# Kernel optimization log

Measured on AMD Instinct MI355X. Metric: run time of the kernel, lower is better.

Reference implementation:

```python
import jax, jax.numpy as jnp
import numpy as np

B, N, Q = 4, 4096, 4096
K = 32                    # max_neighbors (k = min(max_neighbors, N))
NUM_ATOM_TYPES = 100
EMBED_DIM = 32
RBF_DIM = 16
CUTOFF = 5.0
RBF_GAMMA = 1.0 / max(CUTOFF / max(RBF_DIM, 1), 1e-6) ** 2  # 10.24
EPS = 1e-12


def setup_inputs() -> dict:
    key = jax.random.key(0)
    k1, k2, k3, k4, k5 = jax.random.split(key, 5)
    coords = jax.random.normal(k1, (B, N, 3), dtype=jnp.float32) * 10.0
    atom_types = jax.random.randint(k2, (B, N), 0, NUM_ATOM_TYPES)
    radii = jax.random.uniform(k3, (B, N), dtype=jnp.float32) + 0.5
    query_points = jax.random.normal(k4, (B, Q, 3), dtype=jnp.float32) * 10.0
    atom_mask = jnp.ones((B, N), dtype=bool)
    query_mask = jnp.ones((B, Q), dtype=bool)
    embed_table = jax.random.normal(k5, (NUM_ATOM_TYPES, EMBED_DIM), dtype=jnp.float32)
    rbf_centers = jnp.linspace(0.0, CUTOFF, RBF_DIM, dtype=jnp.float32)
    return {"coords": coords, "atom_types": atom_types, "radii": radii,
            "query_points": query_points, "atom_mask": atom_mask,
            "query_mask": query_mask, "embed_table": embed_table,
            "rbf_centers": rbf_centers}


def reference(coords, atom_types, radii, query_points, atom_mask, query_mask,
              embed_table, rbf_centers):
    b = coords.shape[0]
    # stable pairwise distances [B, Q, N]
    diff = query_points[:, :, None, :] - coords[:, None, :, :]
    dists = jnp.sqrt(jnp.sum(diff * diff, axis=-1) + EPS)
    masked_dists = jnp.where(atom_mask[:, None, :], dists, jnp.inf)
    # smallest-k via top_k on negated distances -> [B, Q, K]
    neg_vals, sorted_indices = jax.lax.top_k(-masked_dists, K)
    sorted_dists = -neg_vals

    bidx = jnp.arange(b)[:, None, None]                       # [B,1,1]
    neighbor_atom_mask = atom_mask[bidx, sorted_indices]      # [B,Q,K]
    neighbor_mask = neighbor_atom_mask & (sorted_dists <= CUTOFF) & query_mask[:, :, None]

    neighbor_coords = coords[bidx, sorted_indices]            # [B,Q,K,3]
    neighbor_radii = radii[bidx, sorted_indices][..., None]   # [B,Q,K,1]
    neighbor_types = atom_types[bidx, sorted_indices]         # [B,Q,K]
    neighbor_emb = embed_table[neighbor_types]                # [B,Q,K,E]

    rel_pos = query_points[:, :, None, :] - neighbor_coords   # [B,Q,K,3]
    rel_dist = sorted_dists[..., None]                        # [B,Q,K,1]
    rbf = jnp.exp(-RBF_GAMMA * (rel_dist - rbf_centers[None, None, None, :]) ** 2)

    features = jnp.concatenate([rel_pos, neighbor_radii, neighbor_emb, rbf, rel_dist], axis=-1)
    features = jnp.where(neighbor_mask[..., None], features, 0.0)

    safe_indices = jnp.where(neighbor_atom_mask, sorted_indices, -1)
    safe_dists = jnp.where(neighbor_mask, sorted_dists, 0.0)
    return features, neighbor_mask, safe_indices, safe_dists
```

## Files before the change

### kernel.cpp

```cpp
#include <hip/hip_runtime.h>
#include <stdint.h>

#define B_ 4
#define N_ 4096
#define Q_ 4096
#define K_ 32
#define E_ 32
#define R_ 16
#define F_ 53

static constexpr int WAVES   = 16;
static constexpr int THREADS = WAVES * 64;
static constexpr int SUB     = 1024;
static constexpr int CAPL    = 352;
static constexpr int CAPT    = 64;
static constexpr int TILE    = K_ * F_;
static constexpr int NSLOT   = 4;
static constexpr int POOLB   = NSLOT * TILE * 4;

typedef float v2f __attribute__((ext_vector_type(2)));

__device__ __forceinline__ v2f pk_add(v2f a, v2f b) {
    v2f d; asm("v_pk_add_f32 %0, %1, %2" : "=v"(d) : "v"(a), "v"(b)); return d;
}
__device__ __forceinline__ v2f pk_mul(v2f a, v2f b) {
    v2f d; asm("v_pk_mul_f32 %0, %1, %2" : "=v"(d) : "v"(a), "v"(b)); return d;
}
__device__ __forceinline__ v2f pk_fma(v2f a, v2f b, v2f c) {
    v2f d; asm("v_pk_fma_f32 %0, %1, %2, %3" : "=v"(d) : "v"(a), "v"(b), "v"(c)); return d;
}
__device__ __forceinline__ v2f pk_s2(v2f qx, v2f qy, v2f qz,
                                     v2f nx, v2f ny, v2f nz) {
    const v2f dx = pk_add(qx, nx);
    const v2f dy = pk_add(qy, ny);
    const v2f dz = pk_add(qz, nz);
    return pk_fma(dz, dz, pk_fma(dy, dy, pk_mul(dx, dx)));
}
__device__ __forceinline__ float s2_fma(float qx, float qy, float qz,
                                        float nx, float ny, float nz) {
    const float dx = __fadd_rn(qx, nx);
    const float dy = __fadd_rn(qy, ny);
    const float dz = __fadd_rn(qz, nz);
    return __fmaf_rn(dz, dz, __fmaf_rn(dy, dy, __fmul_rn(dx, dx)));
}

__device__ __forceinline__ void bitonic_sort64_u32(unsigned int& v, int lane) {
    #pragma unroll
    for (int k = 2; k <= 64; k <<= 1) {
        #pragma unroll
        for (int j = k >> 1; j > 0; j >>= 1) {
            unsigned int o = __shfl_xor(v, j);
            const bool asc = ((lane & k) == 0);
            const bool lower = ((lane & j) == 0);
            unsigned int mn = v < o ? v : o;
            unsigned int mx = v < o ? o : v;
            v = (lower == asc) ? mn : mx;
        }
    }
}

__device__ __forceinline__ void bitonic_sort64_u64(unsigned long long& v, int lane) {
    #pragma unroll
    for (int k = 2; k <= 64; k <<= 1) {
        #pragma unroll
        for (int j = k >> 1; j > 0; j >>= 1) {
            unsigned long long o = __shfl_xor(v, j);
            const bool asc = ((lane & k) == 0);
            const bool lower = ((lane & j) == 0);
            unsigned long long mn = v < o ? v : o;
            unsigned long long mx = v < o ? o : v;
            v = (lower == asc) ? mn : mx;
        }
    }
}

__device__ __forceinline__ void merge64_u64(unsigned long long& best,
                                            unsigned long long c, int lane) {
    unsigned long long rev = __shfl(c, 63 - lane);
    unsigned long long v = best < rev ? best : rev;
    #pragma unroll
    for (int j = 32; j > 0; j >>= 1) {
        unsigned long long o = __shfl_xor(v, j);
        const bool lower = ((lane & j) == 0);
        unsigned long long mn = v < o ? v : o;
        unsigned long long mx = v < o ? o : v;
        v = lower ? mn : mx;
    }
    best = v;
}

__global__ __launch_bounds__(THREADS, 8)
void lfb_kernel(const float* __restrict__ coords,
                const int* __restrict__ atom_types,
                const float* __restrict__ radii,
                const float* __restrict__ qpts,
                const int* __restrict__ atom_mask,
                const int* __restrict__ query_mask,
                const float* __restrict__ embed,
                const float* __restrict__ centers,
                float* __restrict__ out)
{
    __shared__ __align__(16) float nsx[N_], nsy[N_], nsz[N_];
    __shared__ __align__(16) unsigned char pool[POOLB];

    const int tid  = threadIdx.x;
    const int lane = tid & 63;
    const int wv   = tid >> 6;
    const int bq0  = blockIdx.x * WAVES;
    const int b    = bq0 / Q_;

    for (int i = tid; i < N_; i += THREADS) {
        const float* c = coords + (size_t)(b * N_ + i) * 3;
        const bool mv = atom_mask[b * N_ + i] != 0;
        nsx[i] = mv ? -c[0] : -1e30f;
        nsy[i] = mv ? -c[1] : -1e30f;
        nsz[i] = mv ? -c[2] : -1e30f;
    }
    __syncthreads();

    const int bq = bq0 + wv;
    const float qx = qpts[(size_t)bq * 3 + 0];
    const float qy = qpts[(size_t)bq * 3 + 1];
    const float qz = qpts[(size_t)bq * 3 + 2];
    const v2f qx2 = {qx, qx}, qy2 = {qy, qy}, qz2 = {qz, qz};

    const float INFf = __uint_as_float(0x7F800000u);

    float l0 = INFf, l1 = INFf, l2 = INFf, l3 = INFf;
    for (int i = 0; i < SUB / 256; ++i) {
        const int a0 = i * 256 + lane * 4;
        const float4 X = *(const float4*)&nsx[a0];
        const float4 Y = *(const float4*)&nsy[a0];
        const float4 Z = *(const float4*)&nsz[a0];
        const v2f Xl = {X.x, X.y}, Xh = {X.z, X.w};
        const v2f Yl = {Y.x, Y.y}, Yh = {Y.z, Y.w};
        const v2f Zl = {Z.x, Z.y}, Zh = {Z.z, Z.w};
        const v2f sl = pk_s2(qx2, qy2, qz2, Xl, Yl, Zl);
        const v2f sh = pk_s2(qx2, qy2, qz2, Xh, Yh, Zh);
        l0 = fminf(l0, sl.x); l1 = fminf(l1, sl.y);
        l2 = fminf(l2, sh.x); l3 = fminf(l3, sh.y);
    }
    unsigned int tsl = __float_as_uint(fminf(fminf(l0, l1), fminf(l2, l3)));
    bitonic_sort64_u32(tsl, lane);
    const unsigned int STl = __shfl(tsl, 31) + 64u;

    unsigned int* loose = reinterpret_cast<unsigned int*>(pool) + wv * CAPL;
    unsigned int* tight = reinterpret_cast<unsigned int*>(pool)
                        + WAVES * CAPL + wv * CAPT;
    const unsigned long long lt = (1ull << lane) - 1ull;
    int cnt = 0;
    float m0 = INFf, m1 = INFf, m2 = INFf, m3 = INFf;
    auto collect = [&](float s, int idx) {
        const bool p = __float_as_uint(s) <= STl;
        const unsigned long long m = __ballot(p);
        if (p) {
            const int sl = cnt + __popcll(m & lt);
            if (sl < CAPL) loose[sl] = (unsigned int)idx;
        }
        cnt += __popcll(m);
    };
    for (int i = 0; i < N_ / 256; ++i) {
        const int a0 = i * 256 + lane * 4;
        const float4 X = *(const float4*)&nsx[a0];
        const float4 Y = *(const float4*)&nsy[a0];
        const float4 Z = *(const float4*)&nsz[a0];
        const v2f Xl = {X.x, X.y}, Xh = {X.z, X.w};
        const v2f Yl = {Y.x, Y.y}, Yh = {Y.z, Y.w};
        const v2f Zl = {Z.x, Z.y}, Zh = {Z.z, Z.w};
        const v2f sl = pk_s2(qx2, qy2, qz2, Xl, Yl, Zl);
        const v2f sh = pk_s2(qx2, qy2, qz2, Xh, Yh, Zh);
        m0 = fminf(m0, sl.x); m1 = fminf(m1, sl.y);
        m2 = fminf(m2, sh.x); m3 = fminf(m3, sh.y);
        collect(sl.x, a0 + 0);
        collect(sl.y, a0 + 1);
        collect(sh.x, a0 + 2);
        collect(sh.y, a0 + 3);
    }
    unsigned int tst = __float_as_uint(fminf(fminf(m0, m1), fminf(m2, m3)));
    bitonic_sort64_u32(tst, lane);
    const unsigned int STt = __shfl(tst, 31) + 64u;

    auto rekey = [&](int id) -> unsigned long long {
        const float dx = __fadd_rn(qx, nsx[id]);
        const float dy = __fadd_rn(qy, nsy[id]);
        const float dz = __fadd_rn(qz, nsz[id]);
        const float sv = __fadd_rn(
            __fadd_rn(__fmul_rn(dx, dx), __fmul_rn(dy, dy)),
            __fmul_rn(dz, dz));
        const float d = __fsqrt_rn(__fadd_rn(sv, 1e-12f));
        return ((unsigned long long)__float_as_uint(d) << 32) | (unsigned int)id;
    };

    unsigned long long key;
    if (cnt <= CAPL) {
        int tcnt = 0;
        const int nchL = (cnt + 63) >> 6;
        for (int c = 0; c < nchL; ++c) {
            const int slot = c * 64 + lane;
            const bool valid = slot < cnt;
            const int id = valid ? (int)loose[slot] : 0;
            const float s = s2_fma(qx, qy, qz, nsx[id], nsy[id], nsz[id]);
            const bool p = valid && (__float_as_uint(s) <= STt);
            const unsigned long long m = __ballot(p);
            if (p) {
                const int sl = tcnt + __popcll(m & lt);
                if (sl < CAPT) tight[sl] = (unsigned int)id;
            }
            tcnt += __popcll(m);
        }
        if (tcnt <= CAPT) {
            unsigned long long v = (lane < tcnt) ? rekey((int)tight[lane]) : ~0ull;
            bitonic_sort64_u64(v, lane);
            key = v;
        } else {
            unsigned long long best = ~0ull;
            for (int c = 0; c < nchL; ++c) {
                const int slot = c * 64 + lane;
                unsigned long long v =
                    (slot < cnt) ? rekey((int)loose[slot]) : ~0ull;
                bitonic_sort64_u64(v, lane);
                if (c == 0) best = v;
                else        merge64_u64(best, v, lane);
            }
            key = best;
        }
    } else {
        key = ~0ull;
        for (int base = 0; base < N_; base += 64) {
            const unsigned long long cand = rekey(base + lane);
            const unsigned long long T = __shfl(key, 31);
            unsigned long long m = __ballot(cand < T);
            while (m) {
                const int src = __ffsll(m) - 1;
                m &= m - 1;
                const unsigned long long nk = __shfl(cand, src);
                const unsigned long long up = __shfl_up(key, 1);
                if (lane < K_) {
                    const unsigned long long repl =
                        (lane == 0) ? nk : (up <= nk ? nk : up);
                    key = (key <= nk) ? key : repl;
                }
            }
        }
    }

    const size_t BQK = (size_t)B_ * Q_ * K_;
    float* out_feat = out;
    float* out_mask = out + BQK * (size_t)F_;
    float* out_idx  = out_mask + BQK;
    float* out_dist = out_idx + BQK;

    const bool qm = query_mask[bq] != 0;

    const float d_l  = __uint_as_float((unsigned int)(key >> 32));
    const int   id_l = (int)(key & 0xFFFFFFFFull) & (N_ - 1);
    const bool  am_l = ((unsigned int)(key >> 32)) < 0x7F800000u;
    const bool  nm_l = am_l && (d_l <= 5.0f) && qm;

    if (lane < K_) {
        const size_t o = (size_t)bq * K_ + lane;
        out_mask[o] = nm_l ? 1.0f : 0.0f;
        out_idx[o]  = am_l ? (float)id_l : -1.0f;
        out_dist[o] = nm_l ? d_l : 0.0f;
    }

    __syncthreads();

    float* stagef = reinterpret_cast<float*>(pool);
    for (int r = 0; r < WAVES / NSLOT; ++r) {
        if ((wv >> 2) == r) {
            float* f0 = stagef + (size_t)(wv & (NSLOT - 1)) * TILE;
            if (lane < K_) {
                float* f = f0 + lane * F_;
                f[0] = nm_l ? __fadd_rn(qx, nsx[id_l]) : 0.0f;
                f[1] = nm_l ? __fadd_rn(qy, nsy[id_l]) : 0.0f;
                f[2] = nm_l ? __fadd_rn(qz, nsz[id_l]) : 0.0f;
                f[3] = nm_l ? radii[b * N_ + id_l] : 0.0f;

                const int t = atom_types[b * N_ + id_l];
                const float4* er4 = (const float4*)(embed + t * E_);
                #pragma unroll
                for (int e = 0; e < E_ / 4; ++e) {
                    const float4 v = er4[e];
                    f[4 + e * 4 + 0] = nm_l ? v.x : 0.0f;
                    f[4 + e * 4 + 1] = nm_l ? v.y : 0.0f;
                    f[4 + e * 4 + 2] = nm_l ? v.z : 0.0f;
                    f[4 + e * 4 + 3] = nm_l ? v.w : 0.0f;
                }

                const float NG = -(float)(256.0 / 25.0);
                #pragma unroll
                for (int rr = 0; rr < R_; ++rr) {
                    const float dd = __fsub_rn(d_l, centers[rr]);
                    const float a2 = __fmul_rn(dd, dd);
                    f[36 + rr] = nm_l ? expf(__fmul_rn(NG, a2)) : 0.0f;
                }
                f[52] = nm_l ? d_l : 0.0f;
            }
            const float4* s4 = (const float4*)f0;
            float4* d4 = (float4*)(out_feat + (size_t)bq * (size_t)TILE);
            for (int t4 = lane; t4 < TILE / 4; t4 += 64) d4[t4] = s4[t4];
        }
        __syncthreads();
    }
}

extern "C" void kernel_launch(void* const* d_in, const int* in_sizes, int n_in,
                              void* d_out, int out_size, void* d_ws, size_t ws_size,
                              hipStream_t stream) {
    const float* coords     = (const float*)d_in[0];
    const int*   atom_types = (const int*)d_in[1];
    const float* radii      = (const float*)d_in[2];
    const float* qpts       = (const float*)d_in[3];
    const int*   atom_mask  = (const int*)d_in[4];
    const int*   query_mask = (const int*)d_in[5];
    const float* embed      = (const float*)d_in[6];
    const float* centers    = (const float*)d_in[7];

    dim3 grid((B_ * Q_) / WAVES);
    dim3 block(THREADS);
    lfb_kernel<<<grid, block, 0, stream>>>(coords, atom_types, radii, qpts,
                                           atom_mask, query_mask, embed, centers,
                                           (float*)d_out);
}
```

Before: 73.22 us.

## Replace two-stage ballot candidate filtering with exact full-scan threshold and per-lane buffers

```diff
diff --git a/kernel.cpp b/kernel.cpp
--- a/kernel.cpp
+++ b/kernel.cpp
@@ -11,12 +11,13 @@
 
 static constexpr int WAVES   = 16;
 static constexpr int THREADS = WAVES * 64;
-static constexpr int SUB     = 1024;
-static constexpr int CAPL    = 352;
-static constexpr int CAPT    = 64;
+static constexpr int CAP     = 6;
+static constexpr int CBUFW   = CAP * 64;
 static constexpr int TILE    = K_ * F_;
 static constexpr int NSLOT   = 4;
-static constexpr int POOLB   = NSLOT * TILE * 4;
+static constexpr int POOLU   = WAVES * CBUFW + WAVES * 64;
+static constexpr int POOLB   = (POOLU * 4 > NSLOT * TILE * 4)
+                             ? (POOLU * 4) : (NSLOT * TILE * 4);
 
 typedef float v2f __attribute__((ext_vector_type(2)));
 
@@ -35,13 +36,6 @@
     const v2f dy = pk_add(qy, ny);
     const v2f dz = pk_add(qz, nz);
     return pk_fma(dz, dz, pk_fma(dy, dy, pk_mul(dx, dx)));
-}
-__device__ __forceinline__ float s2_fma(float qx, float qy, float qz,
-                                        float nx, float ny, float nz) {
-    const float dx = __fadd_rn(qx, nx);
-    const float dy = __fadd_rn(qy, ny);
-    const float dz = __fadd_rn(qz, nz);
-    return __fmaf_rn(dz, dz, __fmaf_rn(dy, dy, __fmul_rn(dx, dx)));
 }
 
 __device__ __forceinline__ void bitonic_sort64_u32(unsigned int& v, int lane) {
@@ -72,21 +66,6 @@
             v = (lower == asc) ? mn : mx;
         }
     }
-}
-
-__device__ __forceinline__ void merge64_u64(unsigned long long& best,
-                                            unsigned long long c, int lane) {
-    unsigned long long rev = __shfl(c, 63 - lane);
-    unsigned long long v = best < rev ? best : rev;
-    #pragma unroll
-    for (int j = 32; j > 0; j >>= 1) {
-        unsigned long long o = __shfl_xor(v, j);
-        const bool lower = ((lane & j) == 0);
-        unsigned long long mn = v < o ? v : o;
-        unsigned long long mx = v < o ? o : v;
-        v = lower ? mn : mx;
-    }
-    best = v;
 }
 
 __global__ __launch_bounds__(THREADS, 8)
@@ -127,7 +106,7 @@
     const float INFf = __uint_as_float(0x7F800000u);
 
     float l0 = INFf, l1 = INFf, l2 = INFf, l3 = INFf;
-    for (int i = 0; i < SUB / 256; ++i) {
+    for (int i = 0; i < N_ / 256; ++i) {
         const int a0 = i * 256 + lane * 4;
         const float4 X = *(const float4*)&nsx[a0];
         const float4 Y = *(const float4*)&nsy[a0];
@@ -140,25 +119,16 @@
         l0 = fminf(l0, sl.x); l1 = fminf(l1, sl.y);
         l2 = fminf(l2, sh.x); l3 = fminf(l3, sh.y);
     }
-    unsigned int tsl = __float_as_uint(fminf(fminf(l0, l1), fminf(l2, l3)));
-    bitonic_sort64_u32(tsl, lane);
-    const unsigned int STl = __shfl(tsl, 31) + 64u;
-
-    unsigned int* loose = reinterpret_cast<unsigned int*>(pool) + wv * CAPL;
-    unsigned int* tight = reinterpret_cast<unsigned int*>(pool)
-                        + WAVES * CAPL + wv * CAPT;
-    const unsigned long long lt = (1ull << lane) - 1ull;
-    int cnt = 0;
-    float m0 = INFf, m1 = INFf, m2 = INFf, m3 = INFf;
-    auto collect = [&](float s, int idx) {
-        const bool p = __float_as_uint(s) <= STl;
-        const unsigned long long m = __ballot(p);
-        if (p) {
-            const int sl = cnt + __popcll(m & lt);
-            if (sl < CAPL) loose[sl] = (unsigned int)idx;
-        }
-        cnt += __popcll(m);
-    };
+    unsigned int mnb = __float_as_uint(fminf(fminf(l0, l1), fminf(l2, l3)));
+    bitonic_sort64_u32(mnb, lane);
+    const unsigned int Ts = __shfl(mnb, 31);
+    const bool degenerate = (Ts + 64u) >= 0x7F800000u;
+    const float STf = __uint_as_float(Ts + 64u);
+
+    unsigned int* poolu = reinterpret_cast<unsigned int*>(pool);
+    unsigned int* cbuf = poolu + wv * CBUFW;
+    unsigned int* comp = poolu + WAVES * CBUFW + wv * 64;
+    int cl = 0;
     for (int i = 0; i < N_ / 256; ++i) {
         const int a0 = i * 256 + lane * 4;
         const float4 X = *(const float4*)&nsx[a0];
@@ -169,16 +139,37 @@
         const v2f Zl = {Z.x, Z.y}, Zh = {Z.z, Z.w};
         const v2f sl = pk_s2(qx2, qy2, qz2, Xl, Yl, Zl);
         const v2f sh = pk_s2(qx2, qy2, qz2, Xh, Yh, Zh);
-        m0 = fminf(m0, sl.x); m1 = fminf(m1, sl.y);
-        m2 = fminf(m2, sh.x); m3 = fminf(m3, sh.y);
-        collect(sl.x, a0 + 0);
-        collect(sl.y, a0 + 1);
-        collect(sh.x, a0 + 2);
-        collect(sh.y, a0 + 3);
-    }
-    unsigned int tst = __float_as_uint(fminf(fminf(m0, m1), fminf(m2, m3)));
-    bitonic_sort64_u32(tst, lane);
-    const unsigned int STt = __shfl(tst, 31) + 64u;
+        {
+            const int s0 = cl < CAP ? cl : CAP - 1;
+            cbuf[s0 * 64 + lane] = (unsigned int)(a0 + 0);
+            cl += (sl.x <= STf) ? 1 : 0;
+        }
+        {
+            const int s1 = cl < CAP ? cl : CAP - 1;
+            cbuf[s1 * 64 + lane] = (unsigned int)(a0 + 1);
+            cl += (sl.y <= STf) ? 1 : 0;
+        }
+        {
+            const int s2 = cl < CAP ? cl : CAP - 1;
+            cbuf[s2 * 64 + lane] = (unsigned int)(a0 + 2);
+            cl += (sh.x <= STf) ? 1 : 0;
+        }
+        {
+            const int s3 = cl < CAP ? cl : CAP - 1;
+            cbuf[s3 * 64 + lane] = (unsigned int)(a0 + 3);
+            cl += (sh.y <= STf) ? 1 : 0;
+        }
+    }
+    const bool ovf = __ballot(cl >= CAP) != 0ull;
+
+    int x = cl;
+    #pragma unroll
+    for (int j = 1; j < 64; j <<= 1) {
+        const int t = __shfl_up(x, j);
+        if (lane >= j) x += t;
+    }
+    const int excl = x - cl;
+    const int tcnt = __shfl(x, 63);
 
     auto rekey = [&](int id) -> unsigned long long {
         const float dx = __fadd_rn(qx, nsx[id]);
@@ -192,38 +183,12 @@
     };
 
     unsigned long long key;
-    if (cnt <= CAPL) {
-        int tcnt = 0;
-        const int nchL = (cnt + 63) >> 6;
-        for (int c = 0; c < nchL; ++c) {
-            const int slot = c * 64 + lane;
-            const bool valid = slot < cnt;
-            const int id = valid ? (int)loose[slot] : 0;
-            const float s = s2_fma(qx, qy, qz, nsx[id], nsy[id], nsz[id]);
-            const bool p = valid && (__float_as_uint(s) <= STt);
-            const unsigned long long m = __ballot(p);
-            if (p) {
-                const int sl = tcnt + __popcll(m & lt);
-                if (sl < CAPT) tight[sl] = (unsigned int)id;
-            }
-            tcnt += __popcll(m);
-        }
-        if (tcnt <= CAPT) {
-            unsigned long long v = (lane < tcnt) ? rekey((int)tight[lane]) : ~0ull;
-            bitonic_sort64_u64(v, lane);
-            key = v;
-        } else {
-            unsigned long long best = ~0ull;
-            for (int c = 0; c < nchL; ++c) {
-                const int slot = c * 64 + lane;
-                unsigned long long v =
-                    (slot < cnt) ? rekey((int)loose[slot]) : ~0ull;
-                bitonic_sort64_u64(v, lane);
-                if (c == 0) best = v;
-                else        merge64_u64(best, v, lane);
-            }
-            key = best;
-        }
+    if (!degenerate && !ovf && tcnt <= 64) {
+        for (int j = 0; j < cl; ++j) comp[excl + j] = cbuf[j * 64 + lane];
+        unsigned long long v = ~0ull;
+        if (lane < tcnt) v = rekey((int)comp[lane]);
+        bitonic_sort64_u64(v, lane);
+        key = v;
     } else {
         key = ~0ull;
         for (int base = 0; base < N_; base += 64) {
```

Measured after the change: 95.77 us. 1.31x slower.

## Replace two-stage loose/tight candidate filter with single full-scan threshold

Applied to the files above, without the earlier changes.

```diff
diff --git a/kernel.cpp b/kernel.cpp
--- a/kernel.cpp
+++ b/kernel.cpp
@@ -11,12 +11,11 @@
 
 static constexpr int WAVES   = 16;
 static constexpr int THREADS = WAVES * 64;
-static constexpr int SUB     = 1024;
-static constexpr int CAPL    = 352;
-static constexpr int CAPT    = 64;
+static constexpr int CAP     = 208;
 static constexpr int TILE    = K_ * F_;
 static constexpr int NSLOT   = 4;
-static constexpr int POOLB   = NSLOT * TILE * 4;
+static constexpr int POOLB   = (WAVES * CAP * 4 > NSLOT * TILE * 4)
+                             ? (WAVES * CAP * 4) : (NSLOT * TILE * 4);
 
 typedef float v2f __attribute__((ext_vector_type(2)));
 
@@ -35,13 +34,6 @@
     const v2f dy = pk_add(qy, ny);
     const v2f dz = pk_add(qz, nz);
     return pk_fma(dz, dz, pk_fma(dy, dy, pk_mul(dx, dx)));
-}
-__device__ __forceinline__ float s2_fma(float qx, float qy, float qz,
-                                        float nx, float ny, float nz) {
-    const float dx = __fadd_rn(qx, nx);
-    const float dy = __fadd_rn(qy, ny);
-    const float dz = __fadd_rn(qz, nz);
-    return __fmaf_rn(dz, dz, __fmaf_rn(dy, dy, __fmul_rn(dx, dx)));
 }
 
 __device__ __forceinline__ void bitonic_sort64_u32(unsigned int& v, int lane) {
@@ -127,7 +119,7 @@
     const float INFf = __uint_as_float(0x7F800000u);
 
     float l0 = INFf, l1 = INFf, l2 = INFf, l3 = INFf;
-    for (int i = 0; i < SUB / 256; ++i) {
+    for (int i = 0; i < N_ / 256; ++i) {
         const int a0 = i * 256 + lane * 4;
         const float4 X = *(const float4*)&nsx[a0];
         const float4 Y = *(const float4*)&nsy[a0];
@@ -140,22 +132,21 @@
         l0 = fminf(l0, sl.x); l1 = fminf(l1, sl.y);
         l2 = fminf(l2, sh.x); l3 = fminf(l3, sh.y);
     }
-    unsigned int tsl = __float_as_uint(fminf(fminf(l0, l1), fminf(l2, l3)));
-    bitonic_sort64_u32(tsl, lane);
-    const unsigned int STl = __shfl(tsl, 31) + 64u;
-
-    unsigned int* loose = reinterpret_cast<unsigned int*>(pool) + wv * CAPL;
-    unsigned int* tight = reinterpret_cast<unsigned int*>(pool)
-                        + WAVES * CAPL + wv * CAPT;
+    unsigned int mnb = __float_as_uint(fminf(fminf(l0, l1), fminf(l2, l3)));
+    bitonic_sort64_u32(mnb, lane);
+    const unsigned int Ts = __shfl(mnb, 31);
+    const bool degenerate = (Ts + 64u) >= 0x7F800000u;
+    const float STf = __uint_as_float(Ts + 64u);
+
+    unsigned int* cb = reinterpret_cast<unsigned int*>(pool) + wv * CAP;
     const unsigned long long lt = (1ull << lane) - 1ull;
     int cnt = 0;
-    float m0 = INFf, m1 = INFf, m2 = INFf, m3 = INFf;
     auto collect = [&](float s, int idx) {
-        const bool p = __float_as_uint(s) <= STl;
+        const bool p = s <= STf;
         const unsigned long long m = __ballot(p);
         if (p) {
             const int sl = cnt + __popcll(m & lt);
-            if (sl < CAPL) loose[sl] = (unsigned int)idx;
+            if (sl < CAP) cb[sl] = (unsigned int)idx;
         }
         cnt += __popcll(m);
     };
@@ -169,16 +160,11 @@
         const v2f Zl = {Z.x, Z.y}, Zh = {Z.z, Z.w};
         const v2f sl = pk_s2(qx2, qy2, qz2, Xl, Yl, Zl);
         const v2f sh = pk_s2(qx2, qy2, qz2, Xh, Yh, Zh);
-        m0 = fminf(m0, sl.x); m1 = fminf(m1, sl.y);
-        m2 = fminf(m2, sh.x); m3 = fminf(m3, sh.y);
         collect(sl.x, a0 + 0);
         collect(sl.y, a0 + 1);
         collect(sh.x, a0 + 2);
         collect(sh.y, a0 + 3);
     }
-    unsigned int tst = __float_as_uint(fminf(fminf(m0, m1), fminf(m2, m3)));
-    bitonic_sort64_u32(tst, lane);
-    const unsigned int STt = __shfl(tst, 31) + 64u;
 
     auto rekey = [&](int id) -> unsigned long long {
         const float dx = __fadd_rn(qx, nsx[id]);
@@ -192,38 +178,18 @@
     };
 
     unsigned long long key;
-    if (cnt <= CAPL) {
-        int tcnt = 0;
-        const int nchL = (cnt + 63) >> 6;
-        for (int c = 0; c < nchL; ++c) {
+    if (!degenerate && cnt <= CAP) {
+        unsigned long long best = ~0ull;
+        const int nch = (cnt + 63) >> 6;
+        for (int c = 0; c < nch; ++c) {
             const int slot = c * 64 + lane;
-            const bool valid = slot < cnt;
-            const int id = valid ? (int)loose[slot] : 0;
-            const float s = s2_fma(qx, qy, qz, nsx[id], nsy[id], nsz[id]);
-            const bool p = valid && (__float_as_uint(s) <= STt);
-            const unsigned long long m = __ballot(p);
-            if (p) {
-                const int sl = tcnt + __popcll(m & lt);
-                if (sl < CAPT) tight[sl] = (unsigned int)id;
-            }
-            tcnt += __popcll(m);
-        }
-        if (tcnt <= CAPT) {
-            unsigned long long v = (lane < tcnt) ? rekey((int)tight[lane]) : ~0ull;
+            unsigned long long v = ~0ull;
+            if (slot < cnt) v = rekey((int)cb[slot]);
             bitonic_sort64_u64(v, lane);
-            key = v;
-        } else {
-            unsigned long long best = ~0ull;
-            for (int c = 0; c < nchL; ++c) {
-                const int slot = c * 64 + lane;
-                unsigned long long v =
-                    (slot < cnt) ? rekey((int)loose[slot]) : ~0ull;
-                bitonic_sort64_u64(v, lane);
-                if (c == 0) best = v;
-                else        merge64_u64(best, v, lane);
-            }
-            key = best;
-        }
+            if (c == 0) best = v;
+            else        merge64_u64(best, v, lane);
+        }
+        key = best;
     } else {
         key = ~0ull;
         for (int base = 0; base < N_; base += 64) {
```

Measured after the change: 66.65 us. 1.1x faster.
